# Kernel optimization log

Measured on AMD Instinct MI355X. Metric: run time of the kernel, lower is better.

## Reference

```python
import jax, jax.numpy as jnp
import numpy as np

BN_EPS = 1e-5


def _bn(x, g, b, m, v):
    # inference-mode BatchNorm1d over channel dim of [B, C, N]
    return g[:, None] * (x - m[:, None]) * jax.lax.rsqrt(v[:, None] + BN_EPS) + b[:, None]


def _conv1x1(w, x):
    # Conv1d kernel_size=1, no bias: [O, C] x [B, C, N] -> [B, O, N]
    return jnp.einsum('oc,bcn->bon', w, x)


def setup_inputs() -> dict:
    key = jax.random.key(0)
    ks = jax.random.split(key, 32)
    B, N = 8, 4096

    def w(k, sh):
        return jax.random.normal(k, sh, jnp.float32) * 0.05

    def bn_params(k, c):
        k0, k1, k2, k3 = jax.random.split(k, 4)
        g = 1.0 + 0.1 * jax.random.normal(k0, (c,), jnp.float32)
        b = 0.1 * jax.random.normal(k1, (c,), jnp.float32)
        m = 0.1 * jax.random.normal(k2, (c,), jnp.float32)
        v = jax.random.uniform(k3, (c,), jnp.float32, 0.5, 1.5)
        return g, b, m, v

    g1, b1, m1, v1 = bn_params(ks[2], 64)
    gq, bq, mq, vq = bn_params(ks[3], 16)
    gk, bk, mk, vk = bn_params(ks[4], 16)
    gv, bv, mv, vv = bn_params(ks[5], 3)

    return {
        'x': jax.random.normal(ks[0], (B, 3, N), jnp.float32),
        'w1': w(ks[6], (64, 3)),
        'g1': g1, 'b1': b1, 'm1': m1, 'v1': v1,
        'w2': w(ks[7], (128, 64)),
        'wq': w(ks[8], (16, 128)),
        'gq': gq, 'bq': bq, 'mq': mq, 'vq': vq,
        'wk': w(ks[9], (16, 128)),
        'gk': gk, 'bk': bk, 'mk': mk, 'vk': vk,
        'wv': w(ks[10], (3, 128)),
        'gv': gv, 'bv': bv, 'mv': mv, 'vv': vv,
        'alpha': 0.1 * jax.random.normal(ks[11], (1,), jnp.float32),
        'offset': 0.1 * jax.random.normal(ks[12], (1,), jnp.float32),
    }


def reference(x, w1, g1, b1, m1, v1, w2,
              wq, gq, bq, mq, vq,
              wk, gk, bk, mk, vk,
              wv, gv, bv, mv, vv,
              alpha, offset):
    # mlp: conv(3->64) -> BN -> ReLU -> conv(64->128)
    feat = _conv1x1(w2, jax.nn.relu(_bn(_conv1x1(w1, x + offset), g1, b1, m1, v1)))  # [B,128,N]
    q = jax.nn.relu(_bn(_conv1x1(wq, feat), gq, bq, mq, vq))  # [B,16,N]
    k = jax.nn.relu(_bn(_conv1x1(wk, feat), gk, bk, mk, vk))  # [B,16,N]
    energy = jnp.einsum('bcn,bcm->bnm', q, k)                 # [B,N,N] (Q^T K)
    sim = jax.nn.softmax(energy, axis=-1)
    # offset-attention: column-wise L1 renormalization
    sim = sim / (1e-9 + sim.sum(axis=1, keepdims=True))
    v_ = jax.nn.relu(_bn(_conv1x1(wv, feat), gv, bv, mv, vv))  # [B,3,N]
    out = jnp.einsum('bcn,bnm->bcm', v_, sim)                  # [B,3,N]
    return alpha * out + x
```

## Files before the change

kernel.cpp:

```cpp
#include <hip/hip_runtime.h>

#define NPTS 4096
#define NB   8
#define BN_EPS 1e-5f
#define LOG2E 1.4426950408889634f
#define SLICES 4

typedef float f32x16 __attribute__((ext_vector_type(16)));
typedef short bf16x8 __attribute__((ext_vector_type(8)));
typedef unsigned short ushort_t;

#if __has_builtin(__builtin_amdgcn_exp2f)
#define EXP2(x) __builtin_amdgcn_exp2f(x)
#else
#define EXP2(x) exp2f(x)
#endif

__device__ __forceinline__ ushort_t f2bf(float f) {
    unsigned u = __builtin_bit_cast(unsigned, f);
    unsigned r = (u + 0x7FFFu + ((u >> 16) & 1u)) >> 16;
    return (ushort_t)r;
}

__global__ __launch_bounds__(64) void k0_prep(
    const float* __restrict__ w1, const float* __restrict__ g1, const float* __restrict__ b1,
    const float* __restrict__ m1, const float* __restrict__ v1,
    const float* __restrict__ w2,
    const float* __restrict__ wq, const float* __restrict__ gq, const float* __restrict__ bq,
    const float* __restrict__ mq, const float* __restrict__ vq,
    const float* __restrict__ wk, const float* __restrict__ gk, const float* __restrict__ bk,
    const float* __restrict__ mk, const float* __restrict__ vk,
    const float* __restrict__ wv, const float* __restrict__ gv, const float* __restrict__ bv,
    const float* __restrict__ mv, const float* __restrict__ vv,
    float* __restrict__ Wc, float* __restrict__ tb,
    float* __restrict__ w1s, float* __restrict__ t1)
{
    const int j = blockIdx.x;
    const int c = threadIdx.x;
    if (j == 35) {
        float s = g1[c] * rsqrtf(v1[c] + BN_EPS);
        w1s[c*3+0] = s * w1[c*3+0];
        w1s[c*3+1] = s * w1[c*3+1];
        w1s[c*3+2] = s * w1[c*3+2];
        t1[c] = b1[c] - s * m1[c];
        return;
    }
    const float* wrow;
    float g, bb, mm, vr, post = 1.f;
    if (j < 16)      { wrow = wq + j*128;      g = gq[j];    bb = bq[j];    mm = mq[j];    vr = vq[j];    post = LOG2E; }
    else if (j < 32) { int t = j-16; wrow = wk + t*128; g = gk[t]; bb = bk[t]; mm = mk[t]; vr = vk[t]; }
    else             { int t = j-32; wrow = wv + t*128; g = gv[t]; bb = bv[t]; mm = mv[t]; vr = vv[t]; }
    const float sbn = g * rsqrtf(vr + BN_EPS);
    float acc = 0.f;
    for (int o = 0; o < 128; ++o) acc += wrow[o] * w2[o*64 + c];
    Wc[j*64 + c] = post * sbn * acc;
    if (c == 0) tb[j] = post * (bb - sbn * mm);
}

__global__ __launch_bounds__(256) void k1_mlp(
    const float* __restrict__ x, const float* __restrict__ offset,
    const float* __restrict__ Wc, const float* __restrict__ tb,
    const float* __restrict__ w1s, const float* __restrict__ t1,
    ushort_t* __restrict__ qbuf, ushort_t* __restrict__ kbuf, float* __restrict__ aux)
{
    const int p = blockIdx.x*256 + threadIdx.x;
    const int b = p >> 12;
    const int n = p & 4095;
    const float off = offset[0];
    const float* xb = x + (size_t)b*3*NPTS + n;
    const float x0 = xb[0] + off, x1 = xb[NPTS] + off, x2 = xb[2*NPTS] + off;

    float acc[35];
#pragma unroll
    for (int j = 0; j < 35; ++j) acc[j] = tb[j];

    for (int c = 0; c < 64; ++c) {
        const float h = fmaxf(
            fmaf(w1s[c*3+0], x0, fmaf(w1s[c*3+1], x1, fmaf(w1s[c*3+2], x2, t1[c]))), 0.f);
        const float* wc = Wc + c;
#pragma unroll
        for (int j = 0; j < 35; ++j) acc[j] = fmaf(wc[j*64], h, acc[j]);
    }

    unsigned qw[8], kw[8];
#pragma unroll
    for (int i = 0; i < 8; ++i) {
        ushort_t qlo = f2bf(fmaxf(acc[2*i],    0.f));
        ushort_t qhi = f2bf(fmaxf(acc[2*i+1],  0.f));
        qw[i] = (unsigned)qlo | ((unsigned)qhi << 16);
        ushort_t klo = f2bf(fmaxf(acc[16+2*i],   0.f));
        ushort_t khi = f2bf(fmaxf(acc[16+2*i+1], 0.f));
        kw[i] = (unsigned)klo | ((unsigned)khi << 16);
    }
    uint4* qd = (uint4*)(qbuf + (size_t)p*16);
    qd[0] = make_uint4(qw[0], qw[1], qw[2], qw[3]);
    qd[1] = make_uint4(qw[4], qw[5], qw[6], qw[7]);
    uint4* kd = (uint4*)(kbuf + (size_t)p*16);
    kd[0] = make_uint4(kw[0], kw[1], kw[2], kw[3]);
    kd[1] = make_uint4(kw[4], kw[5], kw[6], kw[7]);
    float4* ar = (float4*)(aux + (size_t)p*4);
    *ar = make_float4(fmaxf(acc[32], 0.f), fmaxf(acc[33], 0.f), fmaxf(acc[34], 0.f), 0.f);
}

__global__ __launch_bounds__(256) void k2_rowsum(
    const ushort_t* __restrict__ qbuf, const ushort_t* __restrict__ kbuf,
    float* __restrict__ psum)
{
    const int lane = threadIdx.x & 63;
    const int w = blockIdx.x*4 + (threadIdx.x >> 6);
    const int b = w >> 9;
    const int r = w & 511;
    const int nblk = r >> 2;
    const int slice = r & 3;
    const int n0 = nblk * 32;
    const int m0 = slice * 1024;

    const bf16x8 qfrag = *(const bf16x8*)(qbuf + ((size_t)b*NPTS + n0 + (lane & 31))*16 + (lane >> 5)*8);
    const ushort_t* kb = kbuf + ((size_t)b*NPTS + m0 + (lane & 31))*16 + (lane >> 5)*8;

    float rsum = 0.f;
    bf16x8 kf = *(const bf16x8*)kb;
    for (int t = 0; t < 32; ++t) {
        const bf16x8 kcur = kf;
        if (t + 1 < 32) kf = *(const bf16x8*)(kb + (size_t)(t+1)*512);
        f32x16 acc;
#pragma unroll
        for (int i = 0; i < 16; ++i) acc[i] = 0.f;
        acc = __builtin_amdgcn_mfma_f32_32x32x16_bf16(kcur, qfrag, acc, 0, 0, 0);
#pragma unroll
        for (int i = 0; i < 16; ++i) rsum += EXP2(acc[i]);
    }
    rsum += __shfl_xor(rsum, 32);
    if (lane < 32) psum[((size_t)slice*NB + b)*NPTS + n0 + lane] = rsum;
}

__global__ __launch_bounds__(256) void k3_rowred(
    const float* __restrict__ psum, float* __restrict__ aux)
{
    const int p = blockIdx.x*256 + threadIdx.x;
    const int b = p >> 12;
    const int n = p & 4095;
    float s = 0.f;
#pragma unroll
    for (int sl = 0; sl < SLICES; ++sl) s += psum[((size_t)sl*NB + b)*NPTS + n];
    aux[(size_t)p*4 + 3] = 1.0f / s;
}

__global__ __launch_bounds__(256, 4) void k4_colpass(
    const ushort_t* __restrict__ qbuf, const ushort_t* __restrict__ kbuf,
    const float* __restrict__ aux, float* __restrict__ pcol)
{
    const int lane = threadIdx.x & 63;
    const int w = blockIdx.x*4 + (threadIdx.x >> 6);
    const int b = w >> 9;
    const int r = w & 511;
    const int mblk = r >> 2;
    const int slice = r & 3;
    const int m0 = mblk * 32;
    const int n0 = slice * 1024;

    const bf16x8 afrag = *(const bf16x8*)(kbuf + ((size_t)b*NPTS + m0 + (lane & 31))*16 + (lane >> 5)*8);
    const ushort_t* qb = qbuf + ((size_t)b*NPTS + n0 + (lane & 31))*16 + (lane >> 5)*8;
    const float4* auxp = (const float4*)aux + (size_t)b*NPTS + n0 + (lane & 31);

    float S[16], A0[16], A1[16], A2[16];
#pragma unroll
    for (int i = 0; i < 16; ++i) { S[i] = 0.f; A0[i] = 0.f; A1[i] = 0.f; A2[i] = 0.f; }

    bf16x8 qf = *(const bf16x8*)qb;
    float4 ax = auxp[0];
    for (int t = 0; t < 32; ++t) {
        const bf16x8 qcur = qf;
        const float4 axc = ax;
        if (t + 1 < 32) {
            qf = *(const bf16x8*)(qb + (size_t)(t+1)*512);
            ax = auxp[(size_t)(t+1)*32];
        }
        f32x16 acc;
#pragma unroll
        for (int i = 0; i < 16; ++i) acc[i] = 0.f;
        acc = __builtin_amdgcn_mfma_f32_32x32x16_bf16(afrag, qcur, acc, 0, 0, 0);
#pragma unroll
        for (int i = 0; i < 16; ++i) {
            const float wgt = EXP2(acc[i]) * axc.w;
            S[i]  += wgt;
            A0[i] = fmaf(axc.x, wgt, A0[i]);
            A1[i] = fmaf(axc.y, wgt, A1[i]);
            A2[i] = fmaf(axc.z, wgt, A2[i]);
        }
    }

#pragma unroll
    for (int d = 1; d <= 16; d <<= 1) {
#pragma unroll
        for (int i = 0; i < 16; ++i) {
            S[i]  += __shfl_xor(S[i],  d);
            A0[i] += __shfl_xor(A0[i], d);
            A1[i] += __shfl_xor(A1[i], d);
            A2[i] += __shfl_xor(A2[i], d);
        }
    }

    if ((lane & 31) == 0) {
        const int hi = lane >> 5;
        float* base = pcol + (((size_t)b*SLICES + slice)*4)*NPTS;
#pragma unroll
        for (int i = 0; i < 16; ++i) {
            const int m = m0 + (i & 3) + 8*(i >> 2) + 4*hi;
            base[0*NPTS + m] = S[i];
            base[1*NPTS + m] = A0[i];
            base[2*NPTS + m] = A1[i];
            base[3*NPTS + m] = A2[i];
        }
    }
}

__global__ __launch_bounds__(256) void k5_final(
    const float* __restrict__ pcol, const float* __restrict__ x,
    const float* __restrict__ alpha, float* __restrict__ out)
{
    const int p = blockIdx.x*256 + threadIdx.x;
    const int b = p >> 12;
    const int m = p & 4095;
    float s = 0.f, a0 = 0.f, a1 = 0.f, a2 = 0.f;
#pragma unroll
    for (int sl = 0; sl < SLICES; ++sl) {
        const float* base = pcol + (((size_t)b*SLICES + sl)*4)*NPTS;
        s  += base[0*NPTS + m];
        a0 += base[1*NPTS + m];
        a1 += base[2*NPTS + m];
        a2 += base[3*NPTS + m];
    }
    const float sc = alpha[0] / (1e-9f + s);
    const float* xb = x + (size_t)b*3*NPTS + m;
    float* ob = out + (size_t)b*3*NPTS + m;
    ob[0*NPTS] = fmaf(a0, sc, xb[0*NPTS]);
    ob[1*NPTS] = fmaf(a1, sc, xb[1*NPTS]);
    ob[2*NPTS] = fmaf(a2, sc, xb[2*NPTS]);
}

extern "C" void kernel_launch(void* const* d_in, const int* in_sizes, int n_in,
                              void* d_out, int out_size, void* d_ws, size_t ws_size,
                              hipStream_t stream) {
    const float* x      = (const float*)d_in[0];
    const float* w1     = (const float*)d_in[1];
    const float* g1     = (const float*)d_in[2];
    const float* b1     = (const float*)d_in[3];
    const float* m1     = (const float*)d_in[4];
    const float* v1     = (const float*)d_in[5];
    const float* w2     = (const float*)d_in[6];
    const float* wq     = (const float*)d_in[7];
    const float* gq     = (const float*)d_in[8];
    const float* bq     = (const float*)d_in[9];
    const float* mq     = (const float*)d_in[10];
    const float* vq     = (const float*)d_in[11];
    const float* wk     = (const float*)d_in[12];
    const float* gk     = (const float*)d_in[13];
    const float* bk     = (const float*)d_in[14];
    const float* mk     = (const float*)d_in[15];
    const float* vk     = (const float*)d_in[16];
    const float* wv     = (const float*)d_in[17];
    const float* gv     = (const float*)d_in[18];
    const float* bv     = (const float*)d_in[19];
    const float* mv     = (const float*)d_in[20];
    const float* vv     = (const float*)d_in[21];
    const float* alpha  = (const float*)d_in[22];
    const float* offset = (const float*)d_in[23];

    char* ws = (char*)d_ws;
    float*    Wc   = (float*)(ws + 0);
    float*    tb   = (float*)(ws + 16*1024);
    float*    w1s  = (float*)(ws + 32*1024);
    float*    t1   = (float*)(ws + 48*1024);
    ushort_t* qbuf = (ushort_t*)(ws + 64*1024);
    ushort_t* kbuf = (ushort_t*)(ws + 64*1024 + (size_t)1*1024*1024);
    float*    aux  = (float*)(ws + 64*1024 + (size_t)2*1024*1024);
    float*    psum = (float*)(ws + 64*1024 + (size_t)2*1024*1024 + 512*1024);
    float*    pcol = (float*)(ws + 64*1024 + (size_t)3*1024*1024);

    k0_prep<<<dim3(36), dim3(64), 0, stream>>>(
        w1, g1, b1, m1, v1, w2,
        wq, gq, bq, mq, vq,
        wk, gk, bk, mk, vk,
        wv, gv, bv, mv, vv,
        Wc, tb, w1s, t1);

    k1_mlp<<<dim3(128), dim3(256), 0, stream>>>(
        x, offset, Wc, tb, w1s, t1, qbuf, kbuf, aux);

    k2_rowsum<<<dim3(1024), dim3(256), 0, stream>>>(qbuf, kbuf, psum);
    k3_rowred<<<dim3(128), dim3(256), 0, stream>>>(psum, aux);
    k4_colpass<<<dim3(1024), dim3(256), 0, stream>>>(qbuf, kbuf, aux, pcol);
    k5_final<<<dim3(128), dim3(256), 0, stream>>>(pcol, x, alpha, (float*)d_out);
}
```

Before: 180.1 us.

## Shrink column-pass MFMA tiles, add row-sum slices, widen prep and mlp grids

The column pass switches from 32x32x16 to 16x16x32 bf16 MFMA tiles, with the K dimension zero-padded in half the lanes. This cuts per-lane accumulators from 64 to 16 and doubles the number of waves, aiming at higher occupancy and lower register pressure. The row-sum pass splits columns into 8 slices instead of 4, and the prep and mlp kernels spread their work over more threads or blocks. The cost is wasted MFMA throughput on zero-padded K, more partial sums to reduce, and a moved pcol workspace offset.

```diff
diff --git a/kernel.cpp b/kernel.cpp
--- a/kernel.cpp
+++ b/kernel.cpp
@@ -4,9 +4,11 @@
 #define NB   8
 #define BN_EPS 1e-5f
 #define LOG2E 1.4426950408889634f
-#define SLICES 4
+#define RS_SLICES 8
+#define CS_SLICES 4
 
 typedef float f32x16 __attribute__((ext_vector_type(16)));
+typedef float f32x4  __attribute__((ext_vector_type(4)));
 typedef short bf16x8 __attribute__((ext_vector_type(8)));
 typedef unsigned short ushort_t;
 
@@ -22,7 +24,7 @@
     return (ushort_t)r;
 }
 
-__global__ __launch_bounds__(64) void k0_prep(
+__global__ __launch_bounds__(256) void k0_prep(
     const float* __restrict__ w1, const float* __restrict__ g1, const float* __restrict__ b1,
     const float* __restrict__ m1, const float* __restrict__ v1,
     const float* __restrict__ w2,
@@ -36,34 +38,44 @@
     float* __restrict__ w1s, float* __restrict__ t1)
 {
     const int j = blockIdx.x;
-    const int c = threadIdx.x;
+    const int t = threadIdx.x;
     if (j == 35) {
-        float s = g1[c] * rsqrtf(v1[c] + BN_EPS);
-        w1s[c*3+0] = s * w1[c*3+0];
-        w1s[c*3+1] = s * w1[c*3+1];
-        w1s[c*3+2] = s * w1[c*3+2];
-        t1[c] = b1[c] - s * m1[c];
+        if (t < 64) {
+            float s = g1[t] * rsqrtf(v1[t] + BN_EPS);
+            w1s[t*3+0] = s * w1[t*3+0];
+            w1s[t*3+1] = s * w1[t*3+1];
+            w1s[t*3+2] = s * w1[t*3+2];
+            t1[t] = b1[t] - s * m1[t];
+        }
         return;
     }
+    __shared__ float red[256];
+    const int c = t & 63;
+    const int chunk = t >> 6;
     const float* wrow;
     float g, bb, mm, vr, post = 1.f;
     if (j < 16)      { wrow = wq + j*128;      g = gq[j];    bb = bq[j];    mm = mq[j];    vr = vq[j];    post = LOG2E; }
-    else if (j < 32) { int t = j-16; wrow = wk + t*128; g = gk[t]; bb = bk[t]; mm = mk[t]; vr = vk[t]; }
-    else             { int t = j-32; wrow = wv + t*128; g = gv[t]; bb = bv[t]; mm = mv[t]; vr = vv[t]; }
-    const float sbn = g * rsqrtf(vr + BN_EPS);
+    else if (j < 32) { int u = j-16; wrow = wk + u*128; g = gk[u]; bb = bk[u]; mm = mk[u]; vr = vk[u]; }
+    else             { int u = j-32; wrow = wv + u*128; g = gv[u]; bb = bv[u]; mm = mv[u]; vr = vv[u]; }
     float acc = 0.f;
-    for (int o = 0; o < 128; ++o) acc += wrow[o] * w2[o*64 + c];
-    Wc[j*64 + c] = post * sbn * acc;
-    if (c == 0) tb[j] = post * (bb - sbn * mm);
-}
-
-__global__ __launch_bounds__(256) void k1_mlp(
+    for (int o = chunk*32; o < chunk*32 + 32; ++o) acc = fmaf(wrow[o], w2[o*64 + c], acc);
+    red[t] = acc;
+    __syncthreads();
+    if (t < 64) {
+        const float s4 = red[t] + red[64+t] + red[128+t] + red[192+t];
+        const float sbn = g * rsqrtf(vr + BN_EPS);
+        Wc[j*64 + t] = post * sbn * s4;
+        if (t == 0) tb[j] = post * (bb - sbn * mm);
+    }
+}
+
+__global__ __launch_bounds__(128) void k1_mlp(
     const float* __restrict__ x, const float* __restrict__ offset,
     const float* __restrict__ Wc, const float* __restrict__ tb,
     const float* __restrict__ w1s, const float* __restrict__ t1,
     ushort_t* __restrict__ qbuf, ushort_t* __restrict__ kbuf, float* __restrict__ aux)
 {
-    const int p = blockIdx.x*256 + threadIdx.x;
+    const int p = blockIdx.x*128 + threadIdx.x;
     const int b = p >> 12;
     const int n = p & 4095;
     const float off = offset[0];
@@ -102,27 +114,27 @@
     *ar = make_float4(fmaxf(acc[32], 0.f), fmaxf(acc[33], 0.f), fmaxf(acc[34], 0.f), 0.f);
 }
 
-__global__ __launch_bounds__(256) void k2_rowsum(
+__global__ __launch_bounds__(256, 8) void k2_rowsum(
     const ushort_t* __restrict__ qbuf, const ushort_t* __restrict__ kbuf,
     float* __restrict__ psum)
 {
     const int lane = threadIdx.x & 63;
     const int w = blockIdx.x*4 + (threadIdx.x >> 6);
-    const int b = w >> 9;
-    const int r = w & 511;
-    const int nblk = r >> 2;
-    const int slice = r & 3;
+    const int b = w >> 10;
+    const int r = w & 1023;
+    const int nblk = r >> 3;
+    const int slice = r & 7;
     const int n0 = nblk * 32;
-    const int m0 = slice * 1024;
+    const int m0 = slice * 512;
 
     const bf16x8 qfrag = *(const bf16x8*)(qbuf + ((size_t)b*NPTS + n0 + (lane & 31))*16 + (lane >> 5)*8);
     const ushort_t* kb = kbuf + ((size_t)b*NPTS + m0 + (lane & 31))*16 + (lane >> 5)*8;
 
     float rsum = 0.f;
     bf16x8 kf = *(const bf16x8*)kb;
-    for (int t = 0; t < 32; ++t) {
+    for (int t = 0; t < 16; ++t) {
         const bf16x8 kcur = kf;
-        if (t + 1 < 32) kf = *(const bf16x8*)(kb + (size_t)(t+1)*512);
+        if (t + 1 < 16) kf = *(const bf16x8*)(kb + (size_t)(t+1)*512);
         f32x16 acc;
 #pragma unroll
         for (int i = 0; i < 16; ++i) acc[i] = 0.f;
@@ -142,46 +154,53 @@
     const int n = p & 4095;
     float s = 0.f;
 #pragma unroll
-    for (int sl = 0; sl < SLICES; ++sl) s += psum[((size_t)sl*NB + b)*NPTS + n];
+    for (int sl = 0; sl < RS_SLICES; ++sl) s += psum[((size_t)sl*NB + b)*NPTS + n];
     aux[(size_t)p*4 + 3] = 1.0f / s;
 }
 
-__global__ __launch_bounds__(256, 4) void k4_colpass(
+__global__ __launch_bounds__(256, 8) void k4_colpass(
     const ushort_t* __restrict__ qbuf, const ushort_t* __restrict__ kbuf,
     const float* __restrict__ aux, float* __restrict__ pcol)
 {
     const int lane = threadIdx.x & 63;
     const int w = blockIdx.x*4 + (threadIdx.x >> 6);
-    const int b = w >> 9;
-    const int r = w & 511;
-    const int mblk = r >> 2;
+    const int b = w >> 10;
+    const int r = w & 1023;
+    const int mtile = r >> 2;
     const int slice = r & 3;
-    const int m0 = mblk * 32;
+    const int m0 = mtile * 16;
     const int n0 = slice * 1024;
-
-    const bf16x8 afrag = *(const bf16x8*)(kbuf + ((size_t)b*NPTS + m0 + (lane & 31))*16 + (lane >> 5)*8);
-    const ushort_t* qb = qbuf + ((size_t)b*NPTS + n0 + (lane & 31))*16 + (lane >> 5)*8;
-    const float4* auxp = (const float4*)aux + (size_t)b*NPTS + n0 + (lane & 31);
-
-    float S[16], A0[16], A1[16], A2[16];
-#pragma unroll
-    for (int i = 0; i < 16; ++i) { S[i] = 0.f; A0[i] = 0.f; A1[i] = 0.f; A2[i] = 0.f; }
-
-    bf16x8 qf = *(const bf16x8*)qb;
+    const int g = lane >> 4;
+    const int lc = lane & 15;
+
+    const bf16x8 zero8 = {0,0,0,0,0,0,0,0};
+    bf16x8 afrag = zero8;
+    if (g < 2) afrag = *(const bf16x8*)(kbuf + ((size_t)b*NPTS + m0 + lc)*16 + g*8);
+
+    const ushort_t* qb = qbuf + ((size_t)b*NPTS + n0 + lc)*16 + g*8;
+    const float4* auxp = (const float4*)aux + (size_t)b*NPTS + n0 + lc;
+
+    float S[4]  = {0.f,0.f,0.f,0.f};
+    float A0[4] = {0.f,0.f,0.f,0.f};
+    float A1[4] = {0.f,0.f,0.f,0.f};
+    float A2[4] = {0.f,0.f,0.f,0.f};
+
+    bf16x8 qf = zero8;
+    if (g < 2) qf = *(const bf16x8*)qb;
     float4 ax = auxp[0];
-    for (int t = 0; t < 32; ++t) {
+    for (int t = 0; t < 64; ++t) {
         const bf16x8 qcur = qf;
         const float4 axc = ax;
-        if (t + 1 < 32) {
-            qf = *(const bf16x8*)(qb + (size_t)(t+1)*512);
-            ax = auxp[(size_t)(t+1)*32];
-        }
-        f32x16 acc;
-#pragma unroll
-        for (int i = 0; i < 16; ++i) acc[i] = 0.f;
-        acc = __builtin_amdgcn_mfma_f32_32x32x16_bf16(afrag, qcur, acc, 0, 0, 0);
-#pragma unroll
-        for (int i = 0; i < 16; ++i) {
+        if (t + 1 < 64) {
+            if (g < 2) qf = *(const bf16x8*)(qb + (size_t)(t+1)*256);
+            ax = auxp[(size_t)(t+1)*16];
+        }
+        f32x4 acc;
+#pragma unroll
+        for (int i = 0; i < 4; ++i) acc[i] = 0.f;
+        acc = __builtin_amdgcn_mfma_f32_16x16x32_bf16(afrag, qcur, acc, 0, 0, 0);
+#pragma unroll
+        for (int i = 0; i < 4; ++i) {
             const float wgt = EXP2(acc[i]) * axc.w;
             S[i]  += wgt;
             A0[i] = fmaf(axc.x, wgt, A0[i]);
@@ -191,9 +210,9 @@
     }
 
 #pragma unroll
-    for (int d = 1; d <= 16; d <<= 1) {
-#pragma unroll
-        for (int i = 0; i < 16; ++i) {
+    for (int d = 1; d <= 8; d <<= 1) {
+#pragma unroll
+        for (int i = 0; i < 4; ++i) {
             S[i]  += __shfl_xor(S[i],  d);
             A0[i] += __shfl_xor(A0[i], d);
             A1[i] += __shfl_xor(A1[i], d);
@@ -201,12 +220,11 @@
         }
     }
 
-    if ((lane & 31) == 0) {
-        const int hi = lane >> 5;
-        float* base = pcol + (((size_t)b*SLICES + slice)*4)*NPTS;
-#pragma unroll
-        for (int i = 0; i < 16; ++i) {
-            const int m = m0 + (i & 3) + 8*(i >> 2) + 4*hi;
+    if (lc == 0) {
+        float* base = pcol + (((size_t)b*CS_SLICES + slice)*4)*NPTS;
+#pragma unroll
+        for (int i = 0; i < 4; ++i) {
+            const int m = m0 + g*4 + i;
             base[0*NPTS + m] = S[i];
             base[1*NPTS + m] = A0[i];
             base[2*NPTS + m] = A1[i];
@@ -224,8 +242,8 @@
     const int m = p & 4095;
     float s = 0.f, a0 = 0.f, a1 = 0.f, a2 = 0.f;
 #pragma unroll
-    for (int sl = 0; sl < SLICES; ++sl) {
-        const float* base = pcol + (((size_t)b*SLICES + sl)*4)*NPTS;
+    for (int sl = 0; sl < CS_SLICES; ++sl) {
+        const float* base = pcol + (((size_t)b*CS_SLICES + sl)*4)*NPTS;
         s  += base[0*NPTS + m];
         a0 += base[1*NPTS + m];
         a1 += base[2*NPTS + m];
@@ -276,20 +294,20 @@
     ushort_t* kbuf = (ushort_t*)(ws + 64*1024 + (size_t)1*1024*1024);
     float*    aux  = (float*)(ws + 64*1024 + (size_t)2*1024*1024);
     float*    psum = (float*)(ws + 64*1024 + (size_t)2*1024*1024 + 512*1024);
-    float*    pcol = (float*)(ws + 64*1024 + (size_t)3*1024*1024);
-
-    k0_prep<<<dim3(36), dim3(64), 0, stream>>>(
+    float*    pcol = (float*)(ws + 64*1024 + (size_t)4*1024*1024);
+
+    k0_prep<<<dim3(36), dim3(256), 0, stream>>>(
         w1, g1, b1, m1, v1, w2,
         wq, gq, bq, mq, vq,
         wk, gk, bk, mk, vk,
         wv, gv, bv, mv, vv,
         Wc, tb, w1s, t1);
 
-    k1_mlp<<<dim3(128), dim3(256), 0, stream>>>(
+    k1_mlp<<<dim3(256), dim3(128), 0, stream>>>(
         x, offset, Wc, tb, w1s, t1, qbuf, kbuf, aux);
 
-    k2_rowsum<<<dim3(1024), dim3(256), 0, stream>>>(qbuf, kbuf, psum);
+    k2_rowsum<<<dim3(2048), dim3(256), 0, stream>>>(qbuf, kbuf, psum);
     k3_rowred<<<dim3(128), dim3(256), 0, stream>>>(psum, aux);
-    k4_colpass<<<dim3(1024), dim3(256), 0, stream>>>(qbuf, kbuf, aux, pcol);
+    k4_colpass<<<dim3(2048), dim3(256), 0, stream>>>(qbuf, kbuf, aux, pcol);
     k5_final<<<dim3(128), dim3(256), 0, stream>>>(pcol, x, alpha, (float*)d_out);
 }
```

New measurement: 174.6 us. 3.1% less time.
